# Kernel tuning notes

Measured on AMD Instinct MI355X. Metric: run time of the kernel, lower is better.

## Reference

```python
import jax, jax.numpy as jnp
import numpy as np

N, D, E = 16384, 256, 131072  # nodes, feature dim, directed edges (avg sym degree ~16)


def _build_graph(rng):
    # random edges with no self-loops
    r = rng.integers(0, N, E)
    c = (r + 1 + rng.integers(0, N - 1, E)) % N
    e = np.stack([r, c], 1)
    # symmetrize + dedupe + sort == torch sparse coalesce()
    e = np.unique(np.concatenate([e, e[:, ::-1]], 0), axis=0)
    rows, cols = e[:, 0], e[:, 1]
    deg = np.bincount(rows, minlength=N)
    max_deg = int(deg.max())
    off = np.concatenate([[0], np.cumsum(deg)])
    pos = np.arange(rows.shape[0]) - off[rows]
    nbr = np.zeros((N, max_deg), dtype=np.int32)  # padded neighbor lists (CSR rows)
    nbr[rows, pos] = cols
    return nbr, deg.astype(np.int32)


def setup_inputs() -> dict:
    rng = np.random.default_rng(0)
    vertices = jnp.asarray(rng.standard_normal((N, D)).astype(np.float32))
    nbr, deg = _build_graph(rng)
    return {"vertices": vertices, "nbr": jnp.asarray(nbr), "deg": jnp.asarray(deg)}


def _compute_means(vertices, nbr, deg):
    # Sequential greedy edge-based vertex averaging (RelEdgePool phase 1).
    n, d = vertices.shape
    max_deg = nbr.shape[1]
    slot = jnp.arange(max_deg)

    def step(carry, xs):
        unproc, out, c = carry
        i, nbrs_i, deg_i = xs
        valid = slot < deg_i                      # real (non-pad) neighbors
        sel = valid & unproc[nbrs_i]              # unprocessed cluster members (excl. self)
        is_head = unproc[i]                       # vertex starts a new valid cluster
        # mean over unprocessed members; self is always included when head
        s = jnp.einsum('kd,k->d', vertices[nbrs_i], sel.astype(vertices.dtype)) + vertices[i]
        cnt = (jnp.sum(sel) + 1).astype(vertices.dtype)
        mean = s / cnt
        out = out.at[c].set(jnp.where(is_head, mean, out[c]))
        # mark selected members (and self) as processed, only if this is a head
        mark = jnp.zeros(n, bool).at[nbrs_i].max(sel).at[i].set(True)
        unproc = unproc & ~(mark & is_head)
        c = c + is_head.astype(c.dtype)
        return (unproc, out, c), is_head

    init = (jnp.ones(n, dtype=bool), jnp.zeros((n, d), vertices.dtype), jnp.int32(0))
    (_, out, num_clusters), head_mask = jax.lax.scan(
        step, init, (jnp.arange(n), nbr, deg))
    # out[:num_clusters] are the averaged vertices; rows beyond are zero (preallocated buffer,
    # matching the torch code before its final data-dependent slice).
    # head_mask marks vertex_mappings; mean_mappings == arange(num_clusters).
    return out, head_mask, num_clusters


def reference(vertices, nbr, deg):
    return _compute_means(vertices, nbr, deg)
```

## Files before the change

### kernel.cpp

```cpp
#include <hip/hip_runtime.h>
#include <cstdint>
#include <cstddef>

#define NV 16384
#define DD 256
#define BLK 1024
#define PCAP 7
#define HROW 24

__global__ __launch_bounds__(256)
void k_prep(const int* __restrict__ nbr, const int* __restrict__ deg,
            int maxdeg, int n, uint4* __restrict__ pend_g,
            unsigned short* __restrict__ hi_g)
{
    int v = blockIdx.x * 256 + threadIdx.x;
    if (v >= n) return;
    const int b  = v & ~(BLK - 1);
    const int dv = deg[v];
    const int* __restrict__ row = nbr + (size_t)v * (size_t)maxdeg;
    unsigned short* __restrict__ hrow = hi_g + (size_t)v * HROW;
    unsigned w0 = 0, w1 = 0, w2 = 0, w3 = 0;
    int cnt = 0, hic = 0;
    for (int k = 0; k < dv; ++k) {
        int j = row[k];
        if (j > v) {
            if (hic < HROW - 1) hrow[1 + hic] = (unsigned short)j;
            ++hic;
        } else if (j >= b) {
            unsigned val = (unsigned)(j - b);
            switch (cnt) {
                case 0: w0 |= val << 16; break;
                case 1: w1 |= val;       break;
                case 2: w1 |= val << 16; break;
                case 3: w2 |= val;       break;
                case 4: w2 |= val << 16; break;
                case 5: w3 |= val;       break;
                case 6: w3 |= val << 16; break;
                default: break;
            }
            ++cnt;
        }
    }
    hrow[0] = (unsigned short)hic;
    w0 |= (unsigned)(cnt > 0xffff ? 0xffff : cnt);
    uint4 p; p.x = w0; p.y = w1; p.z = w2; p.w = w3;
    pend_g[v] = p;
}

__global__ __launch_bounds__(1024)
void k_mis(const int* __restrict__ nbr, const int* __restrict__ deg,
           int maxdeg, int n,
           const uint4* __restrict__ pend_g, const unsigned short* __restrict__ hi_g,
           int* __restrict__ headlist, float* __restrict__ out_tail)
{
    __shared__ __align__(16) unsigned char st[NV];
    __shared__ int s_ws[16];
    __shared__ int F[3];
    const int t    = threadIdx.x;
    const int lane = t & 63;
    const int wid  = t >> 6;

    ((uint4*)st)[t] = make_uint4(0u, 0u, 0u, 0u);
    if (t < 3) F[t] = 0;
    __syncthreads();

    uint4 pv = make_uint4(0,0,0,0), h0 = pv, h1 = pv, h2 = pv;
    int   dv = 0;
    if (t < n) {
        pv = pend_g[t];
        const uint4* hp = (const uint4*)(hi_g + (size_t)t * HROW);
        h0 = hp[0]; h1 = hp[1]; h2 = hp[2];
        dv = deg[t];
    }
    int r = 0;

    for (int b = 0; b < n; b += BLK) {
        const int v = b + t;
        uint4 pn = make_uint4(0,0,0,0), n0 = pn, n1 = pn, n2 = pn;
        int   dn = 0;
        {
            int vn = b + BLK + t;
            if (vn < n) {
                pn = pend_g[vn];
                const uint4* hp = (const uint4*)(hi_g + (size_t)vn * HROW);
                n0 = hp[0]; n1 = hp[1]; n2 = hp[2];
                dn = deg[vn];
            }
        }

        const int np = pv.x & 0xffff;
        const int e0 = pv.x >> 16,    e1 = pv.y & 0xffff, e2 = pv.y >> 16;
        const int e3 = pv.z & 0xffff, e4 = pv.z >> 16;
        const int e5 = pv.w & 0xffff, e6 = pv.w >> 16;
        const int hic = (int)(h0.x & 0xffff);
        const int* __restrict__ row = nbr + (size_t)v * (size_t)maxdeg;

        int my = (v < n) ? 0 : 2;
        for (;; ++r) {
            if (t == 0) F[(r + 1) % 3] = 0;
            #pragma unroll
            for (int pass = 0; pass < 3; ++pass) {
                if (my == 0) {
                    if (st[v] != 0) { my = 2; }
                    else {
                        bool anyH = false; int undec = 0;
                        if (np <= PCAP) {
                            if (np > 0) { int s = st[b + e0]; anyH |= (s == 1); undec += (s == 0); }
                            if (np > 1) { int s = st[b + e1]; anyH |= (s == 1); undec += (s == 0); }
                            if (np > 2) { int s = st[b + e2]; anyH |= (s == 1); undec += (s == 0); }
                            if (np > 3) { int s = st[b + e3]; anyH |= (s == 1); undec += (s == 0); }
                            if (np > 4) { int s = st[b + e4]; anyH |= (s == 1); undec += (s == 0); }
                            if (np > 5) { int s = st[b + e5]; anyH |= (s == 1); undec += (s == 0); }
                            if (np > 6) { int s = st[b + e6]; anyH |= (s == 1); undec += (s == 0); }
                        } else {
                            for (int k = 0; k < dv; ++k) {
                                int j = row[k];
                                if (j >= b && j < v) {
                                    int s = st[j];
                                    anyH |= (s == 1); undec += (s == 0);
                                }
                            }
                        }
                        if (anyH) { my = 2; }
                        else if (undec == 0) {
                            my = 1;
                            st[v] = 1;
                            if (hic <= HROW - 1) {
                                #define PUSHE(word, sh, i) if ((i) < hic) st[((word) >> (sh)) & 0xffffu] = 2
                                PUSHE(h0.x,16, 0); PUSHE(h0.y, 0, 1); PUSHE(h0.y,16, 2);
                                PUSHE(h0.z, 0, 3); PUSHE(h0.z,16, 4); PUSHE(h0.w, 0, 5);
                                PUSHE(h0.w,16, 6);
                                PUSHE(h1.x, 0, 7); PUSHE(h1.x,16, 8); PUSHE(h1.y, 0, 9);
                                PUSHE(h1.y,16,10); PUSHE(h1.z, 0,11); PUSHE(h1.z,16,12);
                                PUSHE(h1.w, 0,13); PUSHE(h1.w,16,14);
                                PUSHE(h2.x, 0,15); PUSHE(h2.x,16,16); PUSHE(h2.y, 0,17);
                                PUSHE(h2.y,16,18); PUSHE(h2.z, 0,19); PUSHE(h2.z,16,20);
                                PUSHE(h2.w, 0,21); PUSHE(h2.w,16,22);
                                #undef PUSHE
                            } else {
                                for (int k = 0; k < dv; ++k) {
                                    int j = row[k];
                                    if (j > v) st[j] = 2;
                                }
                            }
                        }
                    }
                }
            }
            if (my == 0) F[r % 3] = 1;
            __syncthreads();
            if (F[r % 3] == 0) { ++r; break; }
        }
        pv = pn; h0 = n0; h1 = n1; h2 = n2; dv = dn;
    }

    const int base = t * (NV / 1024);
    int cnt = 0;
    #pragma unroll
    for (int i = 0; i < NV / 1024; ++i) {
        int v = base + i;
        cnt += (v < n && st[v] == 1) ? 1 : 0;
    }
    int c = cnt;
    #pragma unroll
    for (int off = 1; off < 64; off <<= 1) {
        int x = __shfl_up(c, off);
        if (lane >= off) c += x;
    }
    if (lane == 63) s_ws[wid] = c;
    __syncthreads();
    int wexcl = 0, tot = 0;
    #pragma unroll
    for (int w = 0; w < 16; ++w) {
        int s = s_ws[w];
        tot += s;
        if (w < wid) wexcl += s;
    }
    int excl = wexcl + (c - cnt);
    #pragma unroll
    for (int i = 0; i < NV / 1024; ++i) {
        int v = base + i;
        if (v < n && st[v] == 1) { headlist[excl] = v; ++excl; }
    }
    for (int i = t; i < n; i += 1024)
        out_tail[i] = (st[i] == 1) ? 1.0f : 0.0f;
    if (t == 0) out_tail[n] = (float)tot;
}

__global__ __launch_bounds__(256)
void k_owner(const int* __restrict__ nbr, const int* __restrict__ deg,
             int maxdeg, int n,
             const float* __restrict__ hm, int* __restrict__ owner)
{
    int gid = blockIdx.x * 256 + threadIdx.x;
    int v = gid >> 4, l = gid & 15;
    if (v >= n) return;
    if (hm[v] != 0.0f) { if (l == 0) owner[v] = v; return; }
    const int* __restrict__ row = nbr + (size_t)v * (size_t)maxdeg;
    const int dv = deg[v];
    int mn = 0x7fffffff;
    for (int k = l; k < dv; k += 16) {
        int j = row[k];
        if (hm[j] != 0.0f) mn = min(mn, j);
    }
    #pragma unroll
    for (int off = 8; off; off >>= 1) mn = min(mn, __shfl_xor(mn, off, 16));
    if (l == 0) owner[v] = mn;
}

__global__ __launch_bounds__(256)
void k_avg(const float* __restrict__ vert, const int* __restrict__ nbr,
           const int* __restrict__ deg, int maxdeg, int n,
           const int* __restrict__ headlist, const int* __restrict__ owner,
           const float* __restrict__ tail, float* __restrict__ out)
{
    const int w    = (blockIdx.x * 256 + threadIdx.x) >> 6;
    const int lane = threadIdx.x & 63;
    const int tot  = (int)tail[n];
    if (w >= tot) return;
    const int h = headlist[w];

    const int dh = deg[h];
    const int* __restrict__ row = nbr + (size_t)h * (size_t)maxdeg;

    float4 acc = reinterpret_cast<const float4*>(vert + (size_t)h * DD)[lane];
    int cnt = 1;

    for (int k0 = 0; k0 < dh; k0 += 64) {
        int k = k0 + lane;
        int j = (k < dh) ? row[k] : -1;
        bool mem = (j >= 0) && (owner[j] == h);
        unsigned long long m = __ballot(mem);
        cnt += __popcll(m);
        while (m) {
            int bit = __ffsll((long long)m) - 1;
            m &= (m - 1);
            int jj = __shfl(j, bit);
            float4 rr = reinterpret_cast<const float4*>(vert + (size_t)jj * DD)[lane];
            acc.x += rr.x; acc.y += rr.y; acc.z += rr.z; acc.w += rr.w;
        }
    }
    const float inv = 1.0f / (float)cnt;
    float4 res;
    res.x = acc.x * inv; res.y = acc.y * inv;
    res.z = acc.z * inv; res.w = acc.w * inv;
    reinterpret_cast<float4*>(out + (size_t)w * DD)[lane] = res;
}

extern "C" void kernel_launch(void* const* d_in, const int* in_sizes, int n_in,
                              void* d_out, int out_size, void* d_ws, size_t ws_size,
                              hipStream_t stream)
{
    const float* vert = (const float*)d_in[0];
    const int*   nbr  = (const int*)d_in[1];
    const int*   deg  = (const int*)d_in[2];

    const int n      = in_sizes[2];
    const int maxdeg = in_sizes[1] / n;
    const int d      = in_sizes[0] / n;

    int*   owner    = (int*)d_ws;
    int*   headlist = owner + n;
    uint4* pend_g   = (uint4*)(headlist + n);
    unsigned short* hi_g = (unsigned short*)(pend_g + n);

    float* out      = (float*)d_out;
    float* out_tail = out + (size_t)n * (size_t)d;

    hipMemsetAsync(d_out, 0, (size_t)out_size * sizeof(float), stream);

    hipLaunchKernelGGL(k_prep, dim3((n + 255) / 256), dim3(256), 0, stream,
                       nbr, deg, maxdeg, n, pend_g, hi_g);

    hipLaunchKernelGGL(k_mis, dim3(1), dim3(1024), 0, stream,
                       nbr, deg, maxdeg, n, pend_g, hi_g, headlist, out_tail);

    hipLaunchKernelGGL(k_owner, dim3((n * 16 + 255) / 256), dim3(256), 0, stream,
                       nbr, deg, maxdeg, n, out_tail, owner);

    const int blocks = (n * 64 + 255) / 256;
    hipLaunchKernelGGL(k_avg, dim3(blocks), dim3(256), 0, stream,
                       vert, nbr, deg, maxdeg, n, headlist, owner, out_tail, out);
}
```

Before: 89.08 us.

## Shrink MIS block to 256 threads with 4 vertices each, drop output memset

The single-block greedy MIS kernel now runs 256 threads, each handling four vertices of every 1024-vertex chunk, so each barrier spans fewer waves. Head counting now uses packed popcounts over 16-byte shared-memory reads. The full-output memset is removed; the averaging kernel instead writes zero rows for indices past the cluster count. This trades per-thread serial work and register pressure for cheaper block-wide synchronisation in a latency-bound serial kernel, and saves one launch plus a full-buffer write.

```diff
diff --git a/kernel.cpp b/kernel.cpp
--- a/kernel.cpp
+++ b/kernel.cpp
@@ -5,6 +5,8 @@
 #define NV 16384
 #define DD 256
 #define BLK 1024
+#define TPB 256
+#define VPT (BLK / TPB)
 #define PCAP 7
 #define HROW 24
 
@@ -47,119 +49,132 @@
     pend_g[v] = p;
 }
 
-__global__ __launch_bounds__(1024)
+__global__ __launch_bounds__(TPB)
 void k_mis(const int* __restrict__ nbr, const int* __restrict__ deg,
            int maxdeg, int n,
            const uint4* __restrict__ pend_g, const unsigned short* __restrict__ hi_g,
            int* __restrict__ headlist, float* __restrict__ out_tail)
 {
     __shared__ __align__(16) unsigned char st[NV];
-    __shared__ int s_ws[16];
+    __shared__ int s_ws[TPB / 64];
     __shared__ int F[3];
     const int t    = threadIdx.x;
     const int lane = t & 63;
     const int wid  = t >> 6;
 
-    ((uint4*)st)[t] = make_uint4(0u, 0u, 0u, 0u);
+    #pragma unroll
+    for (int i = 0; i < NV / 16 / TPB; ++i)
+        ((uint4*)st)[t + TPB * i] = make_uint4(0u, 0u, 0u, 0u);
     if (t < 3) F[t] = 0;
     __syncthreads();
 
-    uint4 pv = make_uint4(0,0,0,0), h0 = pv, h1 = pv, h2 = pv;
-    int   dv = 0;
-    if (t < n) {
-        pv = pend_g[t];
-        const uint4* hp = (const uint4*)(hi_g + (size_t)t * HROW);
-        h0 = hp[0]; h1 = hp[1]; h2 = hp[2];
-        dv = deg[t];
+    uint4 pv[VPT], a0[VPT], a1[VPT], a2[VPT];
+    int   dv[VPT];
+    #pragma unroll
+    for (int i = 0; i < VPT; ++i) {
+        int v = t + TPB * i;
+        pv[i] = make_uint4(0,0,0,0); a0[i] = a1[i] = a2[i] = pv[i]; dv[i] = 0;
+        if (v < n) {
+            pv[i] = pend_g[v];
+            const uint4* hp = (const uint4*)(hi_g + (size_t)v * HROW);
+            a0[i] = hp[0]; a1[i] = hp[1]; a2[i] = hp[2];
+            dv[i] = deg[v];
+        }
     }
     int r = 0;
 
     for (int b = 0; b < n; b += BLK) {
-        const int v = b + t;
-        uint4 pn = make_uint4(0,0,0,0), n0 = pn, n1 = pn, n2 = pn;
-        int   dn = 0;
-        {
-            int vn = b + BLK + t;
+        uint4 qv[VPT], b0[VPT], b1[VPT], b2[VPT];
+        int   dn[VPT];
+        #pragma unroll
+        for (int i = 0; i < VPT; ++i) {
+            int vn = b + BLK + t + TPB * i;
+            qv[i] = make_uint4(0,0,0,0); b0[i] = b1[i] = b2[i] = qv[i]; dn[i] = 0;
             if (vn < n) {
-                pn = pend_g[vn];
+                qv[i] = pend_g[vn];
                 const uint4* hp = (const uint4*)(hi_g + (size_t)vn * HROW);
-                n0 = hp[0]; n1 = hp[1]; n2 = hp[2];
-                dn = deg[vn];
+                b0[i] = hp[0]; b1[i] = hp[1]; b2[i] = hp[2];
+                dn[i] = deg[vn];
             }
         }
 
-        const int np = pv.x & 0xffff;
-        const int e0 = pv.x >> 16,    e1 = pv.y & 0xffff, e2 = pv.y >> 16;
-        const int e3 = pv.z & 0xffff, e4 = pv.z >> 16;
-        const int e5 = pv.w & 0xffff, e6 = pv.w >> 16;
-        const int hic = (int)(h0.x & 0xffff);
-        const int* __restrict__ row = nbr + (size_t)v * (size_t)maxdeg;
-
-        int my = (v < n) ? 0 : 2;
+        int my[VPT];
+        #pragma unroll
+        for (int i = 0; i < VPT; ++i) my[i] = (b + t + TPB * i < n) ? 0 : 2;
+
         for (;; ++r) {
             if (t == 0) F[(r + 1) % 3] = 0;
             #pragma unroll
             for (int pass = 0; pass < 3; ++pass) {
-                if (my == 0) {
-                    if (st[v] != 0) { my = 2; }
-                    else {
-                        bool anyH = false; int undec = 0;
-                        if (np <= PCAP) {
-                            if (np > 0) { int s = st[b + e0]; anyH |= (s == 1); undec += (s == 0); }
-                            if (np > 1) { int s = st[b + e1]; anyH |= (s == 1); undec += (s == 0); }
-                            if (np > 2) { int s = st[b + e2]; anyH |= (s == 1); undec += (s == 0); }
-                            if (np > 3) { int s = st[b + e3]; anyH |= (s == 1); undec += (s == 0); }
-                            if (np > 4) { int s = st[b + e4]; anyH |= (s == 1); undec += (s == 0); }
-                            if (np > 5) { int s = st[b + e5]; anyH |= (s == 1); undec += (s == 0); }
-                            if (np > 6) { int s = st[b + e6]; anyH |= (s == 1); undec += (s == 0); }
-                        } else {
-                            for (int k = 0; k < dv; ++k) {
-                                int j = row[k];
-                                if (j >= b && j < v) {
-                                    int s = st[j];
-                                    anyH |= (s == 1); undec += (s == 0);
-                                }
+                #pragma unroll
+                for (int i = 0; i < VPT; ++i) {
+                    if (my[i] != 0) continue;
+                    const int v = b + t + TPB * i;
+                    if (st[v] != 0) { my[i] = 2; continue; }
+                    const int np = pv[i].x & 0xffff;
+                    bool anyH = false; int undec = 0;
+                    if (np <= PCAP) {
+                        if (np > 0) { int s = st[b + (pv[i].x >> 16)];      anyH |= (s == 1); undec += (s == 0); }
+                        if (np > 1) { int s = st[b + (pv[i].y & 0xffff)];   anyH |= (s == 1); undec += (s == 0); }
+                        if (np > 2) { int s = st[b + (pv[i].y >> 16)];      anyH |= (s == 1); undec += (s == 0); }
+                        if (np > 3) { int s = st[b + (pv[i].z & 0xffff)];   anyH |= (s == 1); undec += (s == 0); }
+                        if (np > 4) { int s = st[b + (pv[i].z >> 16)];      anyH |= (s == 1); undec += (s == 0); }
+                        if (np > 5) { int s = st[b + (pv[i].w & 0xffff)];   anyH |= (s == 1); undec += (s == 0); }
+                        if (np > 6) { int s = st[b + (pv[i].w >> 16)];      anyH |= (s == 1); undec += (s == 0); }
+                    } else {
+                        const int* __restrict__ row = nbr + (size_t)v * (size_t)maxdeg;
+                        for (int k = 0; k < dv[i]; ++k) {
+                            int j = row[k];
+                            if (j >= b && j < v) {
+                                int s = st[j];
+                                anyH |= (s == 1); undec += (s == 0);
                             }
                         }
-                        if (anyH) { my = 2; }
-                        else if (undec == 0) {
-                            my = 1;
-                            st[v] = 1;
-                            if (hic <= HROW - 1) {
-                                #define PUSHE(word, sh, i) if ((i) < hic) st[((word) >> (sh)) & 0xffffu] = 2
-                                PUSHE(h0.x,16, 0); PUSHE(h0.y, 0, 1); PUSHE(h0.y,16, 2);
-                                PUSHE(h0.z, 0, 3); PUSHE(h0.z,16, 4); PUSHE(h0.w, 0, 5);
-                                PUSHE(h0.w,16, 6);
-                                PUSHE(h1.x, 0, 7); PUSHE(h1.x,16, 8); PUSHE(h1.y, 0, 9);
-                                PUSHE(h1.y,16,10); PUSHE(h1.z, 0,11); PUSHE(h1.z,16,12);
-                                PUSHE(h1.w, 0,13); PUSHE(h1.w,16,14);
-                                PUSHE(h2.x, 0,15); PUSHE(h2.x,16,16); PUSHE(h2.y, 0,17);
-                                PUSHE(h2.y,16,18); PUSHE(h2.z, 0,19); PUSHE(h2.z,16,20);
-                                PUSHE(h2.w, 0,21); PUSHE(h2.w,16,22);
-                                #undef PUSHE
-                            } else {
-                                for (int k = 0; k < dv; ++k) {
-                                    int j = row[k];
-                                    if (j > v) st[j] = 2;
-                                }
+                    }
+                    if (anyH) { my[i] = 2; }
+                    else if (undec == 0) {
+                        my[i] = 1;
+                        st[v] = 1;
+                        const int hic = (int)(a0[i].x & 0xffff);
+                        if (hic <= HROW - 1) {
+                            #define PUSHE(word, sh, k) if ((k) < hic) st[((word) >> (sh)) & 0xffffu] = 2
+                            PUSHE(a0[i].x,16, 0); PUSHE(a0[i].y, 0, 1); PUSHE(a0[i].y,16, 2);
+                            PUSHE(a0[i].z, 0, 3); PUSHE(a0[i].z,16, 4); PUSHE(a0[i].w, 0, 5);
+                            PUSHE(a0[i].w,16, 6);
+                            PUSHE(a1[i].x, 0, 7); PUSHE(a1[i].x,16, 8); PUSHE(a1[i].y, 0, 9);
+                            PUSHE(a1[i].y,16,10); PUSHE(a1[i].z, 0,11); PUSHE(a1[i].z,16,12);
+                            PUSHE(a1[i].w, 0,13); PUSHE(a1[i].w,16,14);
+                            PUSHE(a2[i].x, 0,15); PUSHE(a2[i].x,16,16); PUSHE(a2[i].y, 0,17);
+                            PUSHE(a2[i].y,16,18); PUSHE(a2[i].z, 0,19); PUSHE(a2[i].z,16,20);
+                            PUSHE(a2[i].w, 0,21); PUSHE(a2[i].w,16,22);
+                            #undef PUSHE
+                        } else {
+                            const int* __restrict__ row = nbr + (size_t)v * (size_t)maxdeg;
+                            for (int k = 0; k < dv[i]; ++k) {
+                                int j = row[k];
+                                if (j > v) st[j] = 2;
                             }
                         }
                     }
                 }
             }
-            if (my == 0) F[r % 3] = 1;
+            bool und = (my[0] == 0) | (my[1] == 0) | (my[2] == 0) | (my[3] == 0);
+            if (und) F[r % 3] = 1;
             __syncthreads();
             if (F[r % 3] == 0) { ++r; break; }
         }
-        pv = pn; h0 = n0; h1 = n1; h2 = n2; dv = dn;
-    }
-
-    const int base = t * (NV / 1024);
+        #pragma unroll
+        for (int i = 0; i < VPT; ++i) {
+            pv[i] = qv[i]; a0[i] = b0[i]; a1[i] = b1[i]; a2[i] = b2[i]; dv[i] = dn[i];
+        }
+    }
+
     int cnt = 0;
     #pragma unroll
-    for (int i = 0; i < NV / 1024; ++i) {
-        int v = base + i;
-        cnt += (v < n && st[v] == 1) ? 1 : 0;
+    for (int i = 0; i < 4; ++i) {
+        uint4 q = ((const uint4*)st)[t * 4 + i];
+        cnt += __popc(q.x & 0x01010101u) + __popc(q.y & 0x01010101u)
+             + __popc(q.z & 0x01010101u) + __popc(q.w & 0x01010101u);
     }
     int c = cnt;
     #pragma unroll
@@ -171,19 +186,18 @@
     __syncthreads();
     int wexcl = 0, tot = 0;
     #pragma unroll
-    for (int w = 0; w < 16; ++w) {
+    for (int w = 0; w < TPB / 64; ++w) {
         int s = s_ws[w];
         tot += s;
         if (w < wid) wexcl += s;
     }
     int excl = wexcl + (c - cnt);
-    #pragma unroll
-    for (int i = 0; i < NV / 1024; ++i) {
-        int v = base + i;
-        if (v < n && st[v] == 1) { headlist[excl] = v; ++excl; }
-    }
-    for (int i = t; i < n; i += 1024)
-        out_tail[i] = (st[i] == 1) ? 1.0f : 0.0f;
+    for (int i = 0; i < 64; ++i) {
+        int v = t * 64 + i;
+        if (st[v] == 1) { headlist[excl] = v; ++excl; }
+    }
+    for (int i = t; i < n; i += TPB)
+        out_tail[i] = (float)(st[i] & 1);
     if (t == 0) out_tail[n] = (float)tot;
 }
 
@@ -216,8 +230,12 @@
 {
     const int w    = (blockIdx.x * 256 + threadIdx.x) >> 6;
     const int lane = threadIdx.x & 63;
+    if (w >= n) return;
     const int tot  = (int)tail[n];
-    if (w >= tot) return;
+    if (w >= tot) {
+        reinterpret_cast<float4*>(out + (size_t)w * DD)[lane] = make_float4(0.f, 0.f, 0.f, 0.f);
+        return;
+    }
     const int h = headlist[w];
 
     const int dh = deg[h];
@@ -267,12 +285,10 @@
     float* out      = (float*)d_out;
     float* out_tail = out + (size_t)n * (size_t)d;
 
-    hipMemsetAsync(d_out, 0, (size_t)out_size * sizeof(float), stream);
-
     hipLaunchKernelGGL(k_prep, dim3((n + 255) / 256), dim3(256), 0, stream,
                        nbr, deg, maxdeg, n, pend_g, hi_g);
 
-    hipLaunchKernelGGL(k_mis, dim3(1), dim3(1024), 0, stream,
+    hipLaunchKernelGGL(k_mis, dim3(1), dim3(TPB), 0, stream,
                        nbr, deg, maxdeg, n, pend_g, hi_g, headlist, out_tail);
 
     hipLaunchKernelGGL(k_owner, dim3((n * 16 + 255) / 256), dim3(256), 0, stream,
```

Measured after the change: 152.1 us. 70.7% more time.

## Rework greedy MIS: pull-based state, smaller blocks, wave early-exit, drop memset

Applied to the files above, without the earlier changes.

The single-block greedy cluster-head kernel switches from a push model, where heads mark higher neighbors as excluded, to a pull model. Each vertex now resolves its own state from up to 15 packed lower neighbors and writes it back. It runs with 512 threads over 512-vertex windows, uses 4 inner passes with a per-wave ballot early exit, and vectorises the final counting and tail writes. The output memset is removed, and the averaging kernel now zero-fills rows past the cluster count itself. The aim is to cut barrier rounds and push-write overhead on the serial critical path, at the cost of more windows, each needing at least one barrier.

```diff
diff --git a/kernel.cpp b/kernel.cpp
--- a/kernel.cpp
+++ b/kernel.cpp
@@ -4,162 +4,129 @@
 
 #define NV 16384
 #define DD 256
-#define BLK 1024
-#define PCAP 7
-#define HROW 24
+#define TPB 512
+#define BLK 512
+#define PCAP 15
+#define NPASS 4
 
 __global__ __launch_bounds__(256)
 void k_prep(const int* __restrict__ nbr, const int* __restrict__ deg,
-            int maxdeg, int n, uint4* __restrict__ pend_g,
-            unsigned short* __restrict__ hi_g)
+            int maxdeg, int n, uint4* __restrict__ pend_g)
 {
     int v = blockIdx.x * 256 + threadIdx.x;
     if (v >= n) return;
-    const int b  = v & ~(BLK - 1);
     const int dv = deg[v];
     const int* __restrict__ row = nbr + (size_t)v * (size_t)maxdeg;
-    unsigned short* __restrict__ hrow = hi_g + (size_t)v * HROW;
-    unsigned w0 = 0, w1 = 0, w2 = 0, w3 = 0;
-    int cnt = 0, hic = 0;
+    unsigned ax = 0, ay = 0, az = 0, aw = 0, bx = 0, by = 0, bz = 0, bw = 0;
+    int cnt = 0;
     for (int k = 0; k < dv; ++k) {
         int j = row[k];
-        if (j > v) {
-            if (hic < HROW - 1) hrow[1 + hic] = (unsigned short)j;
-            ++hic;
-        } else if (j >= b) {
-            unsigned val = (unsigned)(j - b);
+        if (j < v) {
+            unsigned e = (unsigned)j;
             switch (cnt) {
-                case 0: w0 |= val << 16; break;
-                case 1: w1 |= val;       break;
-                case 2: w1 |= val << 16; break;
-                case 3: w2 |= val;       break;
-                case 4: w2 |= val << 16; break;
-                case 5: w3 |= val;       break;
-                case 6: w3 |= val << 16; break;
+                case 0:  ax |= e << 16; break;
+                case 1:  ay |= e;       break;
+                case 2:  ay |= e << 16; break;
+                case 3:  az |= e;       break;
+                case 4:  az |= e << 16; break;
+                case 5:  aw |= e;       break;
+                case 6:  aw |= e << 16; break;
+                case 7:  bx |= e;       break;
+                case 8:  bx |= e << 16; break;
+                case 9:  by |= e;       break;
+                case 10: by |= e << 16; break;
+                case 11: bz |= e;       break;
+                case 12: bz |= e << 16; break;
+                case 13: bw |= e;       break;
+                case 14: bw |= e << 16; break;
                 default: break;
             }
             ++cnt;
         }
     }
-    hrow[0] = (unsigned short)hic;
-    w0 |= (unsigned)(cnt > 0xffff ? 0xffff : cnt);
-    uint4 p; p.x = w0; p.y = w1; p.z = w2; p.w = w3;
-    pend_g[v] = p;
-}
-
-__global__ __launch_bounds__(1024)
+    ax |= (unsigned)(cnt > 0xffff ? 0xffff : cnt);
+    uint4 A; A.x = ax; A.y = ay; A.z = az; A.w = aw;
+    uint4 B; B.x = bx; B.y = by; B.z = bz; B.w = bw;
+    pend_g[2 * (size_t)v]     = A;
+    pend_g[2 * (size_t)v + 1] = B;
+}
+
+#define PRB(E, K) { int q = st[(E)]; if ((K) < np) { anyH |= (q == 1); undec += (q == 0); } }
+
+__global__ __launch_bounds__(TPB)
 void k_mis(const int* __restrict__ nbr, const int* __restrict__ deg,
-           int maxdeg, int n,
-           const uint4* __restrict__ pend_g, const unsigned short* __restrict__ hi_g,
+           int maxdeg, int n, const uint4* __restrict__ pend_g,
            int* __restrict__ headlist, float* __restrict__ out_tail)
 {
     __shared__ __align__(16) unsigned char st[NV];
-    __shared__ int s_ws[16];
+    __shared__ int s_ws[TPB / 64];
     __shared__ int F[3];
     const int t    = threadIdx.x;
     const int lane = t & 63;
     const int wid  = t >> 6;
 
-    ((uint4*)st)[t] = make_uint4(0u, 0u, 0u, 0u);
+    #pragma unroll
+    for (int i = 0; i < NV / 16 / TPB; ++i)
+        ((uint4*)st)[t + TPB * i] = make_uint4(0u, 0u, 0u, 0u);
     if (t < 3) F[t] = 0;
     __syncthreads();
 
-    uint4 pv = make_uint4(0,0,0,0), h0 = pv, h1 = pv, h2 = pv;
-    int   dv = 0;
-    if (t < n) {
-        pv = pend_g[t];
-        const uint4* hp = (const uint4*)(hi_g + (size_t)t * HROW);
-        h0 = hp[0]; h1 = hp[1]; h2 = hp[2];
-        dv = deg[t];
-    }
+    uint4 pa = make_uint4(0,0,0,0), pb = pa;
+    if (t < n) { pa = pend_g[2 * (size_t)t]; pb = pend_g[2 * (size_t)t + 1]; }
     int r = 0;
 
     for (int b = 0; b < n; b += BLK) {
-        const int v = b + t;
-        uint4 pn = make_uint4(0,0,0,0), n0 = pn, n1 = pn, n2 = pn;
-        int   dn = 0;
+        uint4 qa = make_uint4(0,0,0,0), qb = qa;
         {
             int vn = b + BLK + t;
-            if (vn < n) {
-                pn = pend_g[vn];
-                const uint4* hp = (const uint4*)(hi_g + (size_t)vn * HROW);
-                n0 = hp[0]; n1 = hp[1]; n2 = hp[2];
-                dn = deg[vn];
-            }
-        }
-
-        const int np = pv.x & 0xffff;
-        const int e0 = pv.x >> 16,    e1 = pv.y & 0xffff, e2 = pv.y >> 16;
-        const int e3 = pv.z & 0xffff, e4 = pv.z >> 16;
-        const int e5 = pv.w & 0xffff, e6 = pv.w >> 16;
-        const int hic = (int)(h0.x & 0xffff);
-        const int* __restrict__ row = nbr + (size_t)v * (size_t)maxdeg;
-
+            if (vn < n) { qa = pend_g[2 * (size_t)vn]; qb = pend_g[2 * (size_t)vn + 1]; }
+        }
+
+        const int v  = b + t;
+        const int np = (int)(pa.x & 0xffffu);
         int my = (v < n) ? 0 : 2;
+        int dvf = 0;
+        if (my == 0 && np > PCAP) dvf = deg[v];
+
         for (;; ++r) {
             if (t == 0) F[(r + 1) % 3] = 0;
-            #pragma unroll
-            for (int pass = 0; pass < 3; ++pass) {
+            for (int pass = 0; pass < NPASS; ++pass) {
                 if (my == 0) {
-                    if (st[v] != 0) { my = 2; }
-                    else {
-                        bool anyH = false; int undec = 0;
-                        if (np <= PCAP) {
-                            if (np > 0) { int s = st[b + e0]; anyH |= (s == 1); undec += (s == 0); }
-                            if (np > 1) { int s = st[b + e1]; anyH |= (s == 1); undec += (s == 0); }
-                            if (np > 2) { int s = st[b + e2]; anyH |= (s == 1); undec += (s == 0); }
-                            if (np > 3) { int s = st[b + e3]; anyH |= (s == 1); undec += (s == 0); }
-                            if (np > 4) { int s = st[b + e4]; anyH |= (s == 1); undec += (s == 0); }
-                            if (np > 5) { int s = st[b + e5]; anyH |= (s == 1); undec += (s == 0); }
-                            if (np > 6) { int s = st[b + e6]; anyH |= (s == 1); undec += (s == 0); }
-                        } else {
-                            for (int k = 0; k < dv; ++k) {
-                                int j = row[k];
-                                if (j >= b && j < v) {
-                                    int s = st[j];
-                                    anyH |= (s == 1); undec += (s == 0);
-                                }
-                            }
-                        }
-                        if (anyH) { my = 2; }
-                        else if (undec == 0) {
-                            my = 1;
-                            st[v] = 1;
-                            if (hic <= HROW - 1) {
-                                #define PUSHE(word, sh, i) if ((i) < hic) st[((word) >> (sh)) & 0xffffu] = 2
-                                PUSHE(h0.x,16, 0); PUSHE(h0.y, 0, 1); PUSHE(h0.y,16, 2);
-                                PUSHE(h0.z, 0, 3); PUSHE(h0.z,16, 4); PUSHE(h0.w, 0, 5);
-                                PUSHE(h0.w,16, 6);
-                                PUSHE(h1.x, 0, 7); PUSHE(h1.x,16, 8); PUSHE(h1.y, 0, 9);
-                                PUSHE(h1.y,16,10); PUSHE(h1.z, 0,11); PUSHE(h1.z,16,12);
-                                PUSHE(h1.w, 0,13); PUSHE(h1.w,16,14);
-                                PUSHE(h2.x, 0,15); PUSHE(h2.x,16,16); PUSHE(h2.y, 0,17);
-                                PUSHE(h2.y,16,18); PUSHE(h2.z, 0,19); PUSHE(h2.z,16,20);
-                                PUSHE(h2.w, 0,21); PUSHE(h2.w,16,22);
-                                #undef PUSHE
-                            } else {
-                                for (int k = 0; k < dv; ++k) {
-                                    int j = row[k];
-                                    if (j > v) st[j] = 2;
-                                }
-                            }
+                    bool anyH = false; int undec = 0;
+                    if (np <= PCAP) {
+                        PRB(pa.x >> 16,      0)
+                        PRB(pa.y & 0xffffu,  1)  PRB(pa.y >> 16,  2)
+                        PRB(pa.z & 0xffffu,  3)  PRB(pa.z >> 16,  4)
+                        PRB(pa.w & 0xffffu,  5)  PRB(pa.w >> 16,  6)
+                        PRB(pb.x & 0xffffu,  7)  PRB(pb.x >> 16,  8)
+                        PRB(pb.y & 0xffffu,  9)  PRB(pb.y >> 16, 10)
+                        PRB(pb.z & 0xffffu, 11)  PRB(pb.z >> 16, 12)
+                        PRB(pb.w & 0xffffu, 13)  PRB(pb.w >> 16, 14)
+                    } else {
+                        const int* __restrict__ row = nbr + (size_t)v * (size_t)maxdeg;
+                        for (int k = 0; k < dvf; ++k) {
+                            int j = row[k];
+                            if (j < v) { int q = st[j]; anyH |= (q == 1); undec += (q == 0); }
                         }
                     }
+                    if (anyH)            { my = 2; st[v] = 2; }
+                    else if (undec == 0) { my = 1; st[v] = 1; }
                 }
+                if (__ballot(my == 0) == 0ULL) break;
             }
             if (my == 0) F[r % 3] = 1;
             __syncthreads();
             if (F[r % 3] == 0) { ++r; break; }
         }
-        pv = pn; h0 = n0; h1 = n1; h2 = n2; dv = dn;
-    }
-
-    const int base = t * (NV / 1024);
+        pa = qa; pb = qb;
+    }
+
     int cnt = 0;
     #pragma unroll
-    for (int i = 0; i < NV / 1024; ++i) {
-        int v = base + i;
-        cnt += (v < n && st[v] == 1) ? 1 : 0;
+    for (int i = 0; i < 2; ++i) {
+        uint4 q = ((const uint4*)st)[t * 2 + i];
+        cnt += __popc(q.x & 0x01010101u) + __popc(q.y & 0x01010101u)
+             + __popc(q.z & 0x01010101u) + __popc(q.w & 0x01010101u);
     }
     int c = cnt;
     #pragma unroll
@@ -171,19 +138,23 @@
     __syncthreads();
     int wexcl = 0, tot = 0;
     #pragma unroll
-    for (int w = 0; w < 16; ++w) {
+    for (int w = 0; w < TPB / 64; ++w) {
         int s = s_ws[w];
         tot += s;
         if (w < wid) wexcl += s;
     }
     int excl = wexcl + (c - cnt);
-    #pragma unroll
-    for (int i = 0; i < NV / 1024; ++i) {
-        int v = base + i;
-        if (v < n && st[v] == 1) { headlist[excl] = v; ++excl; }
-    }
-    for (int i = t; i < n; i += 1024)
-        out_tail[i] = (st[i] == 1) ? 1.0f : 0.0f;
+    for (int i = 0; i < 32; ++i) {
+        int v = t * 32 + i;
+        if (st[v] == 1) { headlist[excl] = v; ++excl; }
+    }
+    for (int i = t; i < NV / 4; i += TPB) {
+        unsigned w = ((const unsigned*)st)[i];
+        float4 f;
+        f.x = (float)(w & 1u);         f.y = (float)((w >> 8) & 1u);
+        f.z = (float)((w >> 16) & 1u); f.w = (float)((w >> 24) & 1u);
+        ((float4*)out_tail)[i] = f;
+    }
     if (t == 0) out_tail[n] = (float)tot;
 }
 
@@ -216,8 +187,12 @@
 {
     const int w    = (blockIdx.x * 256 + threadIdx.x) >> 6;
     const int lane = threadIdx.x & 63;
+    if (w >= n) return;
     const int tot  = (int)tail[n];
-    if (w >= tot) return;
+    if (w >= tot) {
+        reinterpret_cast<float4*>(out + (size_t)w * DD)[lane] = make_float4(0.f, 0.f, 0.f, 0.f);
+        return;
+    }
     const int h = headlist[w];
 
     const int dh = deg[h];
@@ -262,18 +237,15 @@
     int*   owner    = (int*)d_ws;
     int*   headlist = owner + n;
     uint4* pend_g   = (uint4*)(headlist + n);
-    unsigned short* hi_g = (unsigned short*)(pend_g + n);
 
     float* out      = (float*)d_out;
     float* out_tail = out + (size_t)n * (size_t)d;
 
-    hipMemsetAsync(d_out, 0, (size_t)out_size * sizeof(float), stream);
-
     hipLaunchKernelGGL(k_prep, dim3((n + 255) / 256), dim3(256), 0, stream,
-                       nbr, deg, maxdeg, n, pend_g, hi_g);
-
-    hipLaunchKernelGGL(k_mis, dim3(1), dim3(1024), 0, stream,
-                       nbr, deg, maxdeg, n, pend_g, hi_g, headlist, out_tail);
+                       nbr, deg, maxdeg, n, pend_g);
+
+    hipLaunchKernelGGL(k_mis, dim3(1), dim3(TPB), 0, stream,
+                       nbr, deg, maxdeg, n, pend_g, headlist, out_tail);
 
     hipLaunchKernelGGL(k_owner, dim3((n * 16 + 255) / 256), dim3(256), 0, stream,
                        nbr, deg, maxdeg, n, out_tail, owner);
```

Result: slower. 234.1 us (+162.8%).
